# Kernel tuning notes

Hardware: AMD Instinct MI355X
Metric: run time of the kernel (lower is better)

The kernel has to match this reference:

```python
import jax, jax.numpy as jnp
import numpy as np

NEG_SLOPE = 0.2  # PyG GATConv default negative_slope


def _gat_layer(x, src, dst, W, a_src, a_dst, b, num_nodes):
    # x: [N, Fin] -> h: [N, Fout]
    h = x @ W
    # per-node attention logits (heads=1)
    alpha_s = h @ a_src  # [N]
    alpha_d = h @ a_dst  # [N]
    # edge scores e_ij = LeakyReLU(a_src . h_j + a_dst . h_i), j=src, i=dst
    e = alpha_s[src] + alpha_d[dst]
    e = jnp.where(e >= 0, e, NEG_SLOPE * e)
    # segment softmax over edges sharing the same destination node
    e_max = jax.ops.segment_max(e, dst, num_segments=num_nodes)  # [N]
    w = jnp.exp(e - e_max[dst])  # [E]
    denom = jax.ops.segment_sum(w, dst, num_segments=num_nodes)  # [N]
    alpha = w / denom[dst]  # [E]
    # weighted scatter-sum of source messages into destinations
    out = jax.ops.segment_sum(h[src] * alpha[:, None], dst, num_segments=num_nodes)
    return out + b


def _add_self_loops(edge_index, num_nodes):
    loops = jnp.arange(num_nodes, dtype=edge_index.dtype)
    src = jnp.concatenate([edge_index[0], loops])
    dst = jnp.concatenate([edge_index[1], loops])
    return src, dst


def setup_inputs() -> dict:
    key = jax.random.key(0)
    ks = jax.random.split(key, 8)
    N, E, F_in, F_hid, F_out = 50000, 800000, 128, 128, 64
    inp = {
        "node_features": jax.random.normal(ks[0], (N, F_in), dtype=jnp.float32),
        "edge_index": jax.random.randint(ks[1], (2, E), 0, N, dtype=jnp.int32),
        "W1": jax.random.normal(ks[2], (F_in, F_hid), dtype=jnp.float32) / np.sqrt(F_in),
        "a_src1": jax.random.normal(ks[3], (F_hid,), dtype=jnp.float32) / np.sqrt(F_hid),
        "a_dst1": jax.random.normal(ks[4], (F_hid,), dtype=jnp.float32) / np.sqrt(F_hid),
        "b1": jnp.zeros((F_hid,), dtype=jnp.float32),
        "W2": jax.random.normal(ks[5], (F_hid, F_out), dtype=jnp.float32) / np.sqrt(F_hid),
        "a_src2": jax.random.normal(ks[6], (F_out,), dtype=jnp.float32) / np.sqrt(F_out),
        "a_dst2": jax.random.normal(ks[7], (F_out,), dtype=jnp.float32) / np.sqrt(F_out),
        "b2": jnp.zeros((F_out,), dtype=jnp.float32),
    }
    return inp


def reference(node_features, edge_index, W1, a_src1, a_dst1, b1, W2, a_src2, a_dst2, b2):
    num_nodes = node_features.shape[0]
    src, dst = _add_self_loops(edge_index, num_nodes)
    x = _gat_layer(node_features, src, dst, W1, a_src1, a_dst1, b1, num_nodes)
    x = jax.nn.relu(x)
    x = _gat_layer(x, src, dst, W2, a_src2, a_dst2, b2, num_nodes)
    return x
```

## Files before the change

kernel.cpp:

```cpp
#include <hip/hip_runtime.h>
#include <hip/hip_fp16.h>
#include <cstddef>

#define NEG_SLOPE 0.2f
#define TILE 4096
#define CSR_CAP 6144

typedef _Float16 h8 __attribute__((ext_vector_type(8)));
typedef _Float16 h4 __attribute__((ext_vector_type(4)));
typedef float f4 __attribute__((ext_vector_type(4)));

__device__ __forceinline__ float leaky(float x) { return x >= 0.f ? x : NEG_SLOPE * x; }

__device__ __forceinline__ int wave_iscan(int v, int lane) {
#pragma unroll
    for (int off = 1; off < 64; off <<= 1) {
        int t = __shfl_up(v, off);
        if (lane >= off) v += t;
    }
    return v;
}

__global__ __launch_bounds__(256) void prep(
    const float* __restrict__ W1, const float* __restrict__ W2,
    _Float16* __restrict__ W1t, _Float16* __restrict__ W2t,
    int* __restrict__ bfill)
{
    const int b = blockIdx.x;
    const int tid = threadIdx.x;
    if (b == 0) bfill[tid] = 0;
    if (b < 8) {
        for (int i = b * 2048 + tid; i < (b + 1) * 2048; i += 256) {
            int n = i >> 7, k = i & 127;
            W1t[n * 128 + k] = (_Float16)W1[k * 128 + n];
        }
    } else {
        const int bb = b - 8;
        for (int i = bb * 2048 + tid; i < (bb + 1) * 2048; i += 256) {
            int n = i >> 7, k = i & 127;
            W2t[n * 128 + k] = (_Float16)W2[k * 64 + n];
        }
    }
}

__global__ __launch_bounds__(256) void gemm1_scatter(
    const float* __restrict__ x, const _Float16* __restrict__ Wg,
    const float* __restrict__ a_s, const float* __restrict__ a_d,
    _Float16* __restrict__ hh, float* __restrict__ alphaS, float* __restrict__ alphaD,
    int N, int nblk_gemm,
    const int* __restrict__ src, const int* __restrict__ dst,
    int* __restrict__ bfill, unsigned* __restrict__ staging, int cap, int E)
{
    constexpr int K = 128;
    constexpr int LDK = K + 8;
    constexpr int F = 128;
    constexpr int NT = F / 16;

    __shared__ union {
        struct { _Float16 As[64 * LDK]; _Float16 Wt[F * LDK]; } g;
        struct {
            int lcnt[256]; int loff[256]; int gbase[256]; int ws[4];
            unsigned pairs[TILE]; unsigned char bkt[TILE];
        } s;
    } u;

    const int tid = threadIdx.x;

    if (blockIdx.x < (unsigned)nblk_gemm) {
        const int wave = tid >> 6;
        const int lane = tid & 63;
        const int q = lane >> 4;
        const int c = lane & 15;
        const int rowb = blockIdx.x * 64;

        for (int i = tid; i < 64 * (K / 4); i += 256) {
            int r = i >> 5, c4 = i & 31;
            int gr = rowb + r;
            float4 v = (gr < N) ? *(const float4*)(x + (size_t)gr * K + c4 * 4)
                                : make_float4(0.f, 0.f, 0.f, 0.f);
            h4 hv = { (_Float16)v.x, (_Float16)v.y, (_Float16)v.z, (_Float16)v.w };
            *(h4*)(u.g.As + r * LDK + c4 * 4) = hv;
        }
        for (int i = tid; i < F * (K / 8); i += 256) {
            int n = i >> 4, k8 = i & 15;
            *(h8*)(u.g.Wt + n * LDK + k8 * 8) = *(const h8*)(Wg + n * 128 + k8 * 8);
        }
        __syncthreads();

        f4 acc[NT];
#pragma unroll
        for (int nt = 0; nt < NT; nt++) acc[nt] = (f4)0.f;

        const _Float16* aw = u.g.As + (wave * 16 + c) * LDK + q * 8;
#pragma unroll
        for (int kt = 0; kt < 4; kt++) {
            h8 af = *(const h8*)(aw + kt * 32);
#pragma unroll
            for (int nt = 0; nt < NT; nt++) {
                h8 bf = *(const h8*)(u.g.Wt + (nt * 16 + c) * LDK + kt * 32 + q * 8);
                acc[nt] = __builtin_amdgcn_mfma_f32_16x16x32_f16(af, bf, acc[nt], 0, 0, 0);
            }
        }

        float asl[NT], adl[NT];
#pragma unroll
        for (int nt = 0; nt < NT; nt++) {
            asl[nt] = a_s[nt * 16 + c];
            adl[nt] = a_d[nt * 16 + c];
        }
        const int row0 = rowb + wave * 16 + q * 4;
#pragma unroll
        for (int r = 0; r < 4; r++) {
            int row = row0 + r;
            if (row < N) {
                float ps = 0.f, pd = 0.f;
#pragma unroll
                for (int nt = 0; nt < NT; nt++) {
                    float v = acc[nt][r];
                    hh[(size_t)row * F + nt * 16 + c] = (_Float16)v;
                    ps += v * asl[nt];
                    pd += v * adl[nt];
                }
#pragma unroll
                for (int off = 8; off >= 1; off >>= 1) {
                    ps += __shfl_down(ps, off, 16);
                    pd += __shfl_down(pd, off, 16);
                }
                if (c == 0) { alphaS[row] = ps; alphaD[row] = pd; }
            }
        }
    } else {
        const int base = (blockIdx.x - nblk_gemm) * TILE;
        const int vt = min(TILE, E - base);

        u.s.lcnt[tid] = 0;
        __syncthreads();

        int d[TILE / 256], s[TILE / 256], r[TILE / 256];
#pragma unroll
        for (int j = 0; j < TILE / 256; j++) {
            int idx = base + j * 256 + tid;
            if (idx < E) {
                d[j] = dst[idx]; s[j] = src[idx];
                r[j] = atomicAdd(&u.s.lcnt[d[j] >> 8], 1);
            } else d[j] = -1;
        }
        __syncthreads();
        {
            int lane = tid & 63, wid = tid >> 6;
            int v = u.s.lcnt[tid];
            int incl = wave_iscan(v, lane);
            if (lane == 63) u.s.ws[wid] = incl;
            __syncthreads();
            int woff = 0;
            for (int w = 0; w < wid; w++) woff += u.s.ws[w];
            u.s.loff[tid] = woff + incl - v;
        }
        __syncthreads();
        {
            int c = u.s.lcnt[tid];
            if (c > 0) u.s.gbase[tid] = tid * cap + atomicAdd(&bfill[tid], c);
        }
        __syncthreads();
#pragma unroll
        for (int j = 0; j < TILE / 256; j++) {
            if (d[j] >= 0) {
                int b = d[j] >> 8;
                int slot = u.s.loff[b] + r[j];
                u.s.pairs[slot] = ((unsigned)d[j] << 16) | (unsigned)s[j];
                u.s.bkt[slot] = (unsigned char)b;
            }
        }
        __syncthreads();
        for (int slot = tid; slot < vt; slot += 256) {
            int b = u.s.bkt[slot];
            staging[u.s.gbase[b] + (slot - u.s.loff[b])] = u.s.pairs[slot];
        }
    }
}

__global__ __launch_bounds__(1024) void bucket_to_csr(
    const unsigned* __restrict__ staging, const int* __restrict__ bfill,
    int* __restrict__ row_start, int* __restrict__ row_end,
    int* __restrict__ src_sorted, int cap, int N)
{
    __shared__ unsigned lp[CSR_CAP];
    __shared__ int lcnt[256], loff[256], lfill[256];
    __shared__ int ws[4];
    const int tid = threadIdx.x;
    const int b = blockIdx.x;
    const int beg = b * cap;
    const int len = bfill[b];

    if (tid < 256) lcnt[tid] = 0;
    __syncthreads();
    for (int p = tid; p < len; p += 1024) {
        unsigned u = staging[beg + p];
        lp[p] = u;
        atomicAdd(&lcnt[(u >> 16) & 255], 1);
    }
    __syncthreads();
    {
        int lane = tid & 63, wid = tid >> 6;
        int v = 0, incl = 0;
        if (tid < 256) {
            v = lcnt[tid];
            incl = wave_iscan(v, lane);
            if (lane == 63) ws[wid] = incl;
        }
        __syncthreads();
        if (tid < 256) {
            int woff = 0;
            for (int w = 0; w < wid; w++) woff += ws[w];
            int excl = woff + incl - v;
            loff[tid] = excl;
            lfill[tid] = excl;
            int node = (b << 8) + tid;
            if (node < N) { row_start[node] = beg + excl; row_end[node] = beg + excl + v; }
        }
    }
    __syncthreads();
    for (int p = tid; p < len; p += 1024) {
        unsigned u = lp[p];
        int pos = atomicAdd(&lfill[(u >> 16) & 255], 1);
        src_sorted[beg + pos] = (int)(u & 0xFFFFu);
    }
}

__global__ __launch_bounds__(256) void agg1_gemm2(
    const int* __restrict__ row_start, const int* __restrict__ row_end,
    const int* __restrict__ src_sorted, const __half* __restrict__ hh1,
    const float* __restrict__ aS1, const float* __restrict__ aD1,
    const float* __restrict__ b1,
    const _Float16* __restrict__ W2t,
    const float* __restrict__ aS2, const float* __restrict__ aD2,
    _Float16* __restrict__ hh2, float* __restrict__ alphaS2, float* __restrict__ alphaD2,
    int N)
{
    constexpr int K = 128;
    constexpr int LDK = K + 8;
    constexpr int F2 = 64;
    constexpr int NT = F2 / 16;

    __shared__ _Float16 As[64 * LDK];
    __shared__ _Float16 Wt[F2 * LDK];

    const int tid = threadIdx.x;
    const int wave = tid >> 6;
    const int lane = tid & 63;
    const int rowb = blockIdx.x * 64;

    for (int i = tid; i < F2 * (K / 8); i += 256) {
        int n = i >> 4, k8 = i & 15;
        *(h8*)(Wt + n * LDK + k8 * 8) = *(const h8*)(W2t + n * 128 + k8 * 8);
    }

    const int sub = lane >> 4;
    const int l = lane & 15;

    for (int it = 0; it < 16; it++) {
        const int r = wave * 16 + it;
        const int i = rowb + r;
        if (i < N) {
            const float adi = aD1[i];
            const int start = row_start[i];
            const int end = row_end[i];

            float accA[8], accB[8];
#pragma unroll
            for (int q = 0; q < 8; q++) { accA[q] = 0.f; accB[q] = 0.f; }
            float denA = 0.f, denB = 0.f;

            int e = start + sub;
            int s0 = (e + 0 * 4 < end) ? src_sorted[e + 0 * 4] : -1;
            int s1 = (e + 1 * 4 < end) ? src_sorted[e + 1 * 4] : -1;
            int s2 = (e + 2 * 4 < end) ? src_sorted[e + 2 * 4] : -1;
            int s3 = (e + 3 * 4 < end) ? src_sorted[e + 3 * 4] : -1;

            while (s0 >= 0) {
                int eb = e + 16;
                int n0 = (eb + 0 * 4 < end) ? src_sorted[eb + 0 * 4] : -1;
                int n1 = (eb + 1 * 4 < end) ? src_sorted[eb + 1 * 4] : -1;
                int n2 = (eb + 2 * 4 < end) ? src_sorted[eb + 2 * 4] : -1;
                int n3 = (eb + 3 * 4 < end) ? src_sorted[eb + 3 * 4] : -1;

                {
                    float w = __expf(leaky(aS1[s0] + adi));
                    uint4 u = *(const uint4*)(hh1 + (size_t)s0 * 128 + l * 8);
                    const __half2* hp = (const __half2*)&u;
#pragma unroll
                    for (int q = 0; q < 4; q++) {
                        float2 f = __half22float2(hp[q]);
                        accA[q * 2] += w * f.x; accA[q * 2 + 1] += w * f.y;
                    }
                    denA += w;
                }
                if (s1 >= 0) {
                    float w = __expf(leaky(aS1[s1] + adi));
                    uint4 u = *(const uint4*)(hh1 + (size_t)s1 * 128 + l * 8);
                    const __half2* hp = (const __half2*)&u;
#pragma unroll
                    for (int q = 0; q < 4; q++) {
                        float2 f = __half22float2(hp[q]);
                        accB[q * 2] += w * f.x; accB[q * 2 + 1] += w * f.y;
                    }
                    denB += w;
                }
                if (s2 >= 0) {
                    float w = __expf(leaky(aS1[s2] + adi));
                    uint4 u = *(const uint4*)(hh1 + (size_t)s2 * 128 + l * 8);
                    const __half2* hp = (const __half2*)&u;
#pragma unroll
                    for (int q = 0; q < 4; q++) {
                        float2 f = __half22float2(hp[q]);
                        accA[q * 2] += w * f.x; accA[q * 2 + 1] += w * f.y;
                    }
                    denA += w;
                }
                if (s3 >= 0) {
                    float w = __expf(leaky(aS1[s3] + adi));
                    uint4 u = *(const uint4*)(hh1 + (size_t)s3 * 128 + l * 8);
                    const __half2* hp = (const __half2*)&u;
#pragma unroll
                    for (int q = 0; q < 4; q++) {
                        float2 f = __half22float2(hp[q]);
                        accB[q * 2] += w * f.x; accB[q * 2 + 1] += w * f.y;
                    }
                    denB += w;
                }
                e = eb;
                s0 = n0; s1 = n1; s2 = n2; s3 = n3;
            }

            float acc[8];
#pragma unroll
            for (int q = 0; q < 8; q++) acc[q] = accA[q] + accB[q];
            float denom = denA + denB;

#pragma unroll
            for (int off = 32; off >= 16; off >>= 1) {
#pragma unroll
                for (int q = 0; q < 8; q++) acc[q] += __shfl_down(acc[q], off);
                denom += __shfl_down(denom, off);
            }

            if (sub == 0) {
                float wsf = __expf(leaky(aS1[i] + adi));
                uint4 u = *(const uint4*)(hh1 + (size_t)i * 128 + l * 8);
                const __half2* hp = (const __half2*)&u;
                float inv = 1.f / (denom + wsf);
                float4 b0 = *(const float4*)(b1 + l * 8);
                float4 bb1 = *(const float4*)(b1 + l * 8 + 4);
                float o[8];
#pragma unroll
                for (int q = 0; q < 4; q++) {
                    float2 f = __half22float2(hp[q]);
                    o[q * 2]     = (acc[q * 2]     + wsf * f.x) * inv;
                    o[q * 2 + 1] = (acc[q * 2 + 1] + wsf * f.y) * inv;
                }
                o[0] += b0.x; o[1] += b0.y; o[2] += b0.z; o[3] += b0.w;
                o[4] += bb1.x; o[5] += bb1.y; o[6] += bb1.z; o[7] += bb1.w;
                h8 hv;
#pragma unroll
                for (int q = 0; q < 8; q++) hv[q] = (_Float16)fmaxf(o[q], 0.f);
                *(h8*)(As + r * LDK + l * 8) = hv;
            }
        }
    }
    __syncthreads();

    const int q = lane >> 4;
    const int c = lane & 15;

    f4 acc[NT];
#pragma unroll
    for (int nt = 0; nt < NT; nt++) acc[nt] = (f4)0.f;

    const _Float16* aw = As + (wave * 16 + c) * LDK + q * 8;
#pragma unroll
    for (int kt = 0; kt < 4; kt++) {
        h8 af = *(const h8*)(aw + kt * 32);
#pragma unroll
        for (int nt = 0; nt < NT; nt++) {
            h8 bf = *(const h8*)(Wt + (nt * 16 + c) * LDK + kt * 32 + q * 8);
            acc[nt] = __builtin_amdgcn_mfma_f32_16x16x32_f16(af, bf, acc[nt], 0, 0, 0);
        }
    }

    float asl[NT], adl[NT];
#pragma unroll
    for (int nt = 0; nt < NT; nt++) {
        asl[nt] = aS2[nt * 16 + c];
        adl[nt] = aD2[nt * 16 + c];
    }
    const int row0 = rowb + wave * 16 + q * 4;
#pragma unroll
    for (int r = 0; r < 4; r++) {
        int row = row0 + r;
        if (row < N) {
            float ps = 0.f, pd = 0.f;
#pragma unroll
            for (int nt = 0; nt < NT; nt++) {
                float v = acc[nt][r];
                hh2[(size_t)row * F2 + nt * 16 + c] = (_Float16)v;
                ps += v * asl[nt];
                pd += v * adl[nt];
            }
#pragma unroll
            for (int off = 8; off >= 1; off >>= 1) {
                ps += __shfl_down(ps, off, 16);
                pd += __shfl_down(pd, off, 16);
            }
            if (c == 0) { alphaS2[row] = ps; alphaD2[row] = pd; }
        }
    }
}

template <int F, bool RELU, typename OT>
__global__ __launch_bounds__(256) void gat_aggregate(
    const int* __restrict__ row_start, const int* __restrict__ row_end,
    const int* __restrict__ src_sorted, const __half* __restrict__ hh,
    const float* __restrict__ aS, const float* __restrict__ aD,
    const float* __restrict__ bias, OT* __restrict__ out, int N)
{
    constexpr int LPE = F / 8;
    constexpr int EPW = 64 / LPE;

    const int i = blockIdx.x * 4 + (threadIdx.x >> 6);
    if (i >= N) return;
    const int lane = threadIdx.x & 63;
    const int sub = lane / LPE;
    const int l = lane % LPE;

    const float adi = aD[i];
    const int start = row_start[i];
    const int end = row_end[i];

    float accA[8], accB[8];
#pragma unroll
    for (int q = 0; q < 8; q++) { accA[q] = 0.f; accB[q] = 0.f; }
    float denA = 0.f, denB = 0.f;

    int e = start + sub;
    int s0 = (e + 0 * EPW < end) ? src_sorted[e + 0 * EPW] : -1;
    int s1 = (e + 1 * EPW < end) ? src_sorted[e + 1 * EPW] : -1;
    int s2 = (e + 2 * EPW < end) ? src_sorted[e + 2 * EPW] : -1;
    int s3 = (e + 3 * EPW < end) ? src_sorted[e + 3 * EPW] : -1;

    while (s0 >= 0) {
        int eb = e + 4 * EPW;
        int n0 = (eb + 0 * EPW < end) ? src_sorted[eb + 0 * EPW] : -1;
        int n1 = (eb + 1 * EPW < end) ? src_sorted[eb + 1 * EPW] : -1;
        int n2 = (eb + 2 * EPW < end) ? src_sorted[eb + 2 * EPW] : -1;
        int n3 = (eb + 3 * EPW < end) ? src_sorted[eb + 3 * EPW] : -1;

        {
            float w = __expf(leaky(aS[s0] + adi));
            uint4 u = *(const uint4*)(hh + (size_t)s0 * F + l * 8);
            const __half2* hp = (const __half2*)&u;
#pragma unroll
            for (int q = 0; q < 4; q++) {
                float2 f = __half22float2(hp[q]);
                accA[q * 2] += w * f.x; accA[q * 2 + 1] += w * f.y;
            }
            denA += w;
        }
        if (s1 >= 0) {
            float w = __expf(leaky(aS[s1] + adi));
            uint4 u = *(const uint4*)(hh + (size_t)s1 * F + l * 8);
            const __half2* hp = (const __half2*)&u;
#pragma unroll
            for (int q = 0; q < 4; q++) {
                float2 f = __half22float2(hp[q]);
                accB[q * 2] += w * f.x; accB[q * 2 + 1] += w * f.y;
            }
            denB += w;
        }
        if (s2 >= 0) {
            float w = __expf(leaky(aS[s2] + adi));
            uint4 u = *(const uint4*)(hh + (size_t)s2 * F + l * 8);
            const __half2* hp = (const __half2*)&u;
#pragma unroll
            for (int q = 0; q < 4; q++) {
                float2 f = __half22float2(hp[q]);
                accA[q * 2] += w * f.x; accA[q * 2 + 1] += w * f.y;
            }
            denA += w;
        }
        if (s3 >= 0) {
            float w = __expf(leaky(aS[s3] + adi));
            uint4 u = *(const uint4*)(hh + (size_t)s3 * F + l * 8);
            const __half2* hp = (const __half2*)&u;
#pragma unroll
            for (int q = 0; q < 4; q++) {
                float2 f = __half22float2(hp[q]);
                accB[q * 2] += w * f.x; accB[q * 2 + 1] += w * f.y;
            }
            denB += w;
        }
        e = eb;
        s0 = n0; s1 = n1; s2 = n2; s3 = n3;
    }

    float acc[8];
#pragma unroll
    for (int q = 0; q < 8; q++) acc[q] = accA[q] + accB[q];
    float denom = denA + denB;

#pragma unroll
    for (int off = 32; off >= LPE; off >>= 1) {
#pragma unroll
        for (int q = 0; q < 8; q++) acc[q] += __shfl_down(acc[q], off);
        denom += __shfl_down(denom, off);
    }

    if (sub == 0) {
        float wsf = __expf(leaky(aS[i] + adi));
        uint4 u = *(const uint4*)(hh + (size_t)i * F + l * 8);
        const __half2* hp = (const __half2*)&u;
        float inv = 1.f / (denom + wsf);
        float4 b0 = *(const float4*)(bias + l * 8);
        float4 b1 = *(const float4*)(bias + l * 8 + 4);
        float o[8];
#pragma unroll
        for (int q = 0; q < 4; q++) {
            float2 f = __half22float2(hp[q]);
            o[q * 2]     = (acc[q * 2]     + wsf * f.x) * inv;
            o[q * 2 + 1] = (acc[q * 2 + 1] + wsf * f.y) * inv;
        }
        o[0] += b0.x; o[1] += b0.y; o[2] += b0.z; o[3] += b0.w;
        o[4] += b1.x; o[5] += b1.y; o[6] += b1.z; o[7] += b1.w;
        if (RELU) {
#pragma unroll
            for (int q = 0; q < 8; q++) o[q] = fmaxf(o[q], 0.f);
        }
        if constexpr (sizeof(OT) == 2) {
            __half2 qh[4];
            qh[0] = __floats2half2_rn(o[0], o[1]);
            qh[1] = __floats2half2_rn(o[2], o[3]);
            qh[2] = __floats2half2_rn(o[4], o[5]);
            qh[3] = __floats2half2_rn(o[6], o[7]);
            *(uint4*)((__half*)out + (size_t)i * F + l * 8) = *(uint4*)qh;
        } else {
            *(float4*)((float*)out + (size_t)i * F + l * 8)     = make_float4(o[0], o[1], o[2], o[3]);
            *(float4*)((float*)out + (size_t)i * F + l * 8 + 4) = make_float4(o[4], o[5], o[6], o[7]);
        }
    }
}

extern "C" void kernel_launch(void* const* d_in, const int* in_sizes, int n_in,
                              void* d_out, int out_size, void* d_ws, size_t ws_size,
                              hipStream_t stream)
{
    const float* x   = (const float*)d_in[0];
    const int*   ei  = (const int*)d_in[1];
    const float* W1  = (const float*)d_in[2];
    const float* aS1 = (const float*)d_in[3];
    const float* aD1 = (const float*)d_in[4];
    const float* b1  = (const float*)d_in[5];
    const float* W2  = (const float*)d_in[6];
    const float* aS2 = (const float*)d_in[7];
    const float* aD2 = (const float*)d_in[8];
    const float* b2  = (const float*)d_in[9];

    const int K = 128, F1 = 128, F2 = 64;
    const int N = in_sizes[0] / K;
    const int E = in_sizes[1] / 2;
    const int* src = ei;
    const int* dst = ei + E;

    const int Np = (N + 4) & ~3;
    const int NB = (N + 255) >> 8;
    const int nbt = (E + TILE - 1) / TILE;
    const int nblk_gemm = (N + 63) / 64;
    int cap = (((E / NB) * 3) / 2 + 255) & ~255;
    if (cap > CSR_CAP) cap = CSR_CAP;

    char* wsb = (char*)d_ws;
    int* bfill        = (int*)wsb;      wsb += 256 * 4;
    _Float16* W1t     = (_Float16*)wsb; wsb += 128 * 128 * 2;
    _Float16* W2t     = (_Float16*)wsb; wsb += 64 * 128 * 2;
    int* row_start    = (int*)wsb;      wsb += (size_t)Np * 4;
    int* row_end      = (int*)wsb;      wsb += (size_t)Np * 4;
    unsigned* staging = (unsigned*)wsb; wsb += (size_t)NB * CSR_CAP * 4;
    int* src_sorted   = (int*)wsb;      wsb += (size_t)NB * CSR_CAP * 4;
    _Float16* hh1     = (_Float16*)wsb; wsb += (size_t)N * F1 * 2;
    _Float16* hh2     = (_Float16*)wsb; wsb += (size_t)N * F2 * 2;
    float* as_        = (float*)wsb;    wsb += (size_t)Np * 4;
    float* ad_        = (float*)wsb;    wsb += (size_t)Np * 4;
    float* as2_       = (float*)wsb;    wsb += (size_t)Np * 4;
    float* ad2_       = (float*)wsb;    wsb += (size_t)Np * 4;

    dim3 blk(256);

    prep<<<dim3(12), blk, 0, stream>>>(W1, W2, W1t, W2t, bfill);

    gemm1_scatter<<<dim3(nblk_gemm + nbt), blk, 0, stream>>>(
        x, W1t, aS1, aD1, hh1, as_, ad_, N, nblk_gemm,
        src, dst, bfill, staging, cap, E);

    bucket_to_csr<<<dim3(NB), dim3(1024), 0, stream>>>(staging, bfill, row_start, row_end,
                                                       src_sorted, cap, N);

    agg1_gemm2<<<dim3(nblk_gemm), blk, 0, stream>>>(
        row_start, row_end, src_sorted, (const __half*)hh1, as_, ad_, b1,
        W2t, aS2, aD2, hh2, as2_, ad2_, N);

    gat_aggregate<F2, false, float><<<dim3((N + 3) / 4), blk, 0, stream>>>(
        row_start, row_end, src_sorted, (const __half*)hh2, as2_, ad2_, b2,
        (float*)d_out, N);
}
```

Measured before the change: 202.0 us.

## Aggregate one node per wave and replace MFMA tile GEMM with scalar dot

The fused layer-1 aggregation plus layer-2 GEMM kernel now gives each block 4 nodes (one per wave) instead of 64 rows with 16 serial aggregations per wave. This gives far more blocks and better latency hiding for the gathers. The 128x64 projection is now done with FP32 scalar FMAs: each wave takes a 32-wide K slice, reads W2t straight from global memory, and partial sums are reduced through shared memory. The MFMA path is dropped. Separately, the bucket_to_csr block size is cut from 1024 to 512 threads.

```diff
diff --git a/kernel.cpp b/kernel.cpp
--- a/kernel.cpp
+++ b/kernel.cpp
@@ -179,7 +179,7 @@
     }
 }
 
-__global__ __launch_bounds__(1024) void bucket_to_csr(
+__global__ __launch_bounds__(512) void bucket_to_csr(
     const unsigned* __restrict__ staging, const int* __restrict__ bfill,
     int* __restrict__ row_start, int* __restrict__ row_end,
     int* __restrict__ src_sorted, int cap, int N)
@@ -194,7 +194,7 @@
 
     if (tid < 256) lcnt[tid] = 0;
     __syncthreads();
-    for (int p = tid; p < len; p += 1024) {
+    for (int p = tid; p < len; p += 512) {
         unsigned u = staging[beg + p];
         lp[p] = u;
         atomicAdd(&lcnt[(u >> 16) & 255], 1);
@@ -220,14 +220,14 @@
         }
     }
     __syncthreads();
-    for (int p = tid; p < len; p += 1024) {
+    for (int p = tid; p < len; p += 512) {
         unsigned u = lp[p];
         int pos = atomicAdd(&lfill[(u >> 16) & 255], 1);
         src_sorted[beg + pos] = (int)(u & 0xFFFFu);
     }
 }
 
-__global__ __launch_bounds__(256) void agg1_gemm2(
+__global__ __launch_bounds__(256) void agg1_gemm2f(
     const int* __restrict__ row_start, const int* __restrict__ row_end,
     const int* __restrict__ src_sorted, const __half* __restrict__ hh1,
     const float* __restrict__ aS1, const float* __restrict__ aD1,
@@ -237,181 +237,154 @@
     _Float16* __restrict__ hh2, float* __restrict__ alphaS2, float* __restrict__ alphaD2,
     int N)
 {
-    constexpr int K = 128;
-    constexpr int LDK = K + 8;
-    constexpr int F2 = 64;
-    constexpr int NT = F2 / 16;
-
-    __shared__ _Float16 As[64 * LDK];
-    __shared__ _Float16 Wt[F2 * LDK];
-
-    const int tid = threadIdx.x;
-    const int wave = tid >> 6;
-    const int lane = tid & 63;
-    const int rowb = blockIdx.x * 64;
-
-    for (int i = tid; i < F2 * (K / 8); i += 256) {
-        int n = i >> 4, k8 = i & 15;
-        *(h8*)(Wt + n * LDK + k8 * 8) = *(const h8*)(W2t + n * 128 + k8 * 8);
-    }
-
+    __shared__ float x2r[4][128];
+    __shared__ float part[4][4][64];
+
+    const int wave = threadIdx.x >> 6;
+    const int lane = threadIdx.x & 63;
+    const int i = blockIdx.x * 4 + wave;
     const int sub = lane >> 4;
     const int l = lane & 15;
 
-    for (int it = 0; it < 16; it++) {
-        const int r = wave * 16 + it;
-        const int i = rowb + r;
-        if (i < N) {
-            const float adi = aD1[i];
-            const int start = row_start[i];
-            const int end = row_end[i];
-
-            float accA[8], accB[8];
-#pragma unroll
-            for (int q = 0; q < 8; q++) { accA[q] = 0.f; accB[q] = 0.f; }
-            float denA = 0.f, denB = 0.f;
-
-            int e = start + sub;
-            int s0 = (e + 0 * 4 < end) ? src_sorted[e + 0 * 4] : -1;
-            int s1 = (e + 1 * 4 < end) ? src_sorted[e + 1 * 4] : -1;
-            int s2 = (e + 2 * 4 < end) ? src_sorted[e + 2 * 4] : -1;
-            int s3 = (e + 3 * 4 < end) ? src_sorted[e + 3 * 4] : -1;
-
-            while (s0 >= 0) {
-                int eb = e + 16;
-                int n0 = (eb + 0 * 4 < end) ? src_sorted[eb + 0 * 4] : -1;
-                int n1 = (eb + 1 * 4 < end) ? src_sorted[eb + 1 * 4] : -1;
-                int n2 = (eb + 2 * 4 < end) ? src_sorted[eb + 2 * 4] : -1;
-                int n3 = (eb + 3 * 4 < end) ? src_sorted[eb + 3 * 4] : -1;
-
-                {
-                    float w = __expf(leaky(aS1[s0] + adi));
-                    uint4 u = *(const uint4*)(hh1 + (size_t)s0 * 128 + l * 8);
-                    const __half2* hp = (const __half2*)&u;
-#pragma unroll
-                    for (int q = 0; q < 4; q++) {
-                        float2 f = __half22float2(hp[q]);
-                        accA[q * 2] += w * f.x; accA[q * 2 + 1] += w * f.y;
-                    }
-                    denA += w;
-                }
-                if (s1 >= 0) {
-                    float w = __expf(leaky(aS1[s1] + adi));
-                    uint4 u = *(const uint4*)(hh1 + (size_t)s1 * 128 + l * 8);
-                    const __half2* hp = (const __half2*)&u;
-#pragma unroll
-                    for (int q = 0; q < 4; q++) {
-                        float2 f = __half22float2(hp[q]);
-                        accB[q * 2] += w * f.x; accB[q * 2 + 1] += w * f.y;
-                    }
-                    denB += w;
-                }
-                if (s2 >= 0) {
-                    float w = __expf(leaky(aS1[s2] + adi));
-                    uint4 u = *(const uint4*)(hh1 + (size_t)s2 * 128 + l * 8);
-                    const __half2* hp = (const __half2*)&u;
-#pragma unroll
-                    for (int q = 0; q < 4; q++) {
-                        float2 f = __half22float2(hp[q]);
-                        accA[q * 2] += w * f.x; accA[q * 2 + 1] += w * f.y;
-                    }
-                    denA += w;
-                }
-                if (s3 >= 0) {
-                    float w = __expf(leaky(aS1[s3] + adi));
-                    uint4 u = *(const uint4*)(hh1 + (size_t)s3 * 128 + l * 8);
-                    const __half2* hp = (const __half2*)&u;
-#pragma unroll
-                    for (int q = 0; q < 4; q++) {
-                        float2 f = __half22float2(hp[q]);
-                        accB[q * 2] += w * f.x; accB[q * 2 + 1] += w * f.y;
-                    }
-                    denB += w;
-                }
-                e = eb;
-                s0 = n0; s1 = n1; s2 = n2; s3 = n3;
-            }
-
-            float acc[8];
-#pragma unroll
-            for (int q = 0; q < 8; q++) acc[q] = accA[q] + accB[q];
-            float denom = denA + denB;
-
-#pragma unroll
-            for (int off = 32; off >= 16; off >>= 1) {
-#pragma unroll
-                for (int q = 0; q < 8; q++) acc[q] += __shfl_down(acc[q], off);
-                denom += __shfl_down(denom, off);
-            }
-
-            if (sub == 0) {
-                float wsf = __expf(leaky(aS1[i] + adi));
-                uint4 u = *(const uint4*)(hh1 + (size_t)i * 128 + l * 8);
+    if (i < N) {
+        const float adi = aD1[i];
+        const int start = row_start[i];
+        const int end = row_end[i];
+
+        float accA[8], accB[8];
+#pragma unroll
+        for (int q = 0; q < 8; q++) { accA[q] = 0.f; accB[q] = 0.f; }
+        float denA = 0.f, denB = 0.f;
+
+        int e = start + sub;
+        int s0 = (e + 0 * 4 < end) ? src_sorted[e + 0 * 4] : -1;
+        int s1 = (e + 1 * 4 < end) ? src_sorted[e + 1 * 4] : -1;
+        int s2 = (e + 2 * 4 < end) ? src_sorted[e + 2 * 4] : -1;
+        int s3 = (e + 3 * 4 < end) ? src_sorted[e + 3 * 4] : -1;
+
+        while (s0 >= 0) {
+            int eb = e + 16;
+            int n0 = (eb + 0 * 4 < end) ? src_sorted[eb + 0 * 4] : -1;
+            int n1 = (eb + 1 * 4 < end) ? src_sorted[eb + 1 * 4] : -1;
+            int n2 = (eb + 2 * 4 < end) ? src_sorted[eb + 2 * 4] : -1;
+            int n3 = (eb + 3 * 4 < end) ? src_sorted[eb + 3 * 4] : -1;
+
+            {
+                float w = __expf(leaky(aS1[s0] + adi));
+                uint4 u = *(const uint4*)(hh1 + (size_t)s0 * 128 + l * 8);
                 const __half2* hp = (const __half2*)&u;
-                float inv = 1.f / (denom + wsf);
-                float4 b0 = *(const float4*)(b1 + l * 8);
-                float4 bb1 = *(const float4*)(b1 + l * 8 + 4);
-                float o[8];
 #pragma unroll
                 for (int q = 0; q < 4; q++) {
                     float2 f = __half22float2(hp[q]);
-                    o[q * 2]     = (acc[q * 2]     + wsf * f.x) * inv;
-                    o[q * 2 + 1] = (acc[q * 2 + 1] + wsf * f.y) * inv;
+                    accA[q * 2] += w * f.x; accA[q * 2 + 1] += w * f.y;
                 }
-                o[0] += b0.x; o[1] += b0.y; o[2] += b0.z; o[3] += b0.w;
-                o[4] += bb1.x; o[5] += bb1.y; o[6] += bb1.z; o[7] += bb1.w;
-                h8 hv;
-#pragma unroll
-                for (int q = 0; q < 8; q++) hv[q] = (_Float16)fmaxf(o[q], 0.f);
-                *(h8*)(As + r * LDK + l * 8) = hv;
-            }
+                denA += w;
+            }
+            if (s1 >= 0) {
+                float w = __expf(leaky(aS1[s1] + adi));
+                uint4 u = *(const uint4*)(hh1 + (size_t)s1 * 128 + l * 8);
+                const __half2* hp = (const __half2*)&u;
+#pragma unroll
+                for (int q = 0; q < 4; q++) {
+                    float2 f = __half22float2(hp[q]);
+                    accB[q * 2] += w * f.x; accB[q * 2 + 1] += w * f.y;
+                }
+                denB += w;
+            }
+            if (s2 >= 0) {
+                float w = __expf(leaky(aS1[s2] + adi));
+                uint4 u = *(const uint4*)(hh1 + (size_t)s2 * 128 + l * 8);
+                const __half2* hp = (const __half2*)&u;
+#pragma unroll
+                for (int q = 0; q < 4; q++) {
+                    float2 f = __half22float2(hp[q]);
+                    accA[q * 2] += w * f.x; accA[q * 2 + 1] += w * f.y;
+                }
+                denA += w;
+            }
+            if (s3 >= 0) {
+                float w = __expf(leaky(aS1[s3] + adi));
+                uint4 u = *(const uint4*)(hh1 + (size_t)s3 * 128 + l * 8);
+                const __half2* hp = (const __half2*)&u;
+#pragma unroll
+                for (int q = 0; q < 4; q++) {
+                    float2 f = __half22float2(hp[q]);
+                    accB[q * 2] += w * f.x; accB[q * 2 + 1] += w * f.y;
+                }
+                denB += w;
+            }
+            e = eb;
+            s0 = n0; s1 = n1; s2 = n2; s3 = n3;
+        }
+
+        float acc[8];
+#pragma unroll
+        for (int q = 0; q < 8; q++) acc[q] = accA[q] + accB[q];
+        float denom = denA + denB;
+
+#pragma unroll
+        for (int off = 32; off >= 16; off >>= 1) {
+#pragma unroll
+            for (int q = 0; q < 8; q++) acc[q] += __shfl_down(acc[q], off);
+            denom += __shfl_down(denom, off);
+        }
+
+        if (sub == 0) {
+            float wsf = __expf(leaky(aS1[i] + adi));
+            uint4 u = *(const uint4*)(hh1 + (size_t)i * 128 + l * 8);
+            const __half2* hp = (const __half2*)&u;
+            float inv = 1.f / (denom + wsf);
+            float4 b0 = *(const float4*)(b1 + l * 8);
+            float4 bb = *(const float4*)(b1 + l * 8 + 4);
+            float o[8];
+#pragma unroll
+            for (int q = 0; q < 4; q++) {
+                float2 f = __half22float2(hp[q]);
+                o[q * 2]     = (acc[q * 2]     + wsf * f.x) * inv;
+                o[q * 2 + 1] = (acc[q * 2 + 1] + wsf * f.y) * inv;
+            }
+            o[0] += b0.x; o[1] += b0.y; o[2] += b0.z; o[3] += b0.w;
+            o[4] += bb.x; o[5] += bb.y; o[6] += bb.z; o[7] += bb.w;
+#pragma unroll
+            for (int q = 0; q < 8; q++) x2r[wave][l * 8 + q] = fmaxf(o[q], 0.f);
         }
     }
     __syncthreads();
 
-    const int q = lane >> 4;
-    const int c = lane & 15;
-
-    f4 acc[NT];
-#pragma unroll
-    for (int nt = 0; nt < NT; nt++) acc[nt] = (f4)0.f;
-
-    const _Float16* aw = As + (wave * 16 + c) * LDK + q * 8;
-#pragma unroll
-    for (int kt = 0; kt < 4; kt++) {
-        h8 af = *(const h8*)(aw + kt * 32);
-#pragma unroll
-        for (int nt = 0; nt < NT; nt++) {
-            h8 bf = *(const h8*)(Wt + (nt * 16 + c) * LDK + kt * 32 + q * 8);
-            acc[nt] = __builtin_amdgcn_mfma_f32_16x16x32_f16(af, bf, acc[nt], 0, 0, 0);
-        }
-    }
-
-    float asl[NT], adl[NT];
-#pragma unroll
-    for (int nt = 0; nt < NT; nt++) {
-        asl[nt] = aS2[nt * 16 + c];
-        adl[nt] = aD2[nt * 16 + c];
-    }
-    const int row0 = rowb + wave * 16 + q * 4;
-#pragma unroll
-    for (int r = 0; r < 4; r++) {
-        int row = row0 + r;
-        if (row < N) {
-            float ps = 0.f, pd = 0.f;
-#pragma unroll
-            for (int nt = 0; nt < NT; nt++) {
-                float v = acc[nt][r];
-                hh2[(size_t)row * F2 + nt * 16 + c] = (_Float16)v;
-                ps += v * asl[nt];
-                pd += v * adl[nt];
-            }
-#pragma unroll
-            for (int off = 8; off >= 1; off >>= 1) {
-                ps += __shfl_down(ps, off, 16);
-                pd += __shfl_down(pd, off, 16);
-            }
-            if (c == 0) { alphaS2[row] = ps; alphaD2[row] = pd; }
+    float p[4] = {0.f, 0.f, 0.f, 0.f};
+#pragma unroll
+    for (int half = 0; half < 2; half++) {
+        const int k0 = wave * 32 + half * 16;
+        h8 wa = *(const h8*)(W2t + lane * 128 + k0);
+        h8 wb = *(const h8*)(W2t + lane * 128 + k0 + 8);
+#pragma unroll
+        for (int m = 0; m < 4; m++) {
+            float s = 0.f;
+#pragma unroll
+            for (int j = 0; j < 8; j++) s += x2r[m][k0 + j] * (float)wa[j];
+#pragma unroll
+            for (int j = 0; j < 8; j++) s += x2r[m][k0 + 8 + j] * (float)wb[j];
+            p[m] += s;
+        }
+    }
+#pragma unroll
+    for (int m = 0; m < 4; m++) part[wave][m][lane] = p[m];
+    __syncthreads();
+
+    {
+        const int m = wave;
+        const int node = blockIdx.x * 4 + m;
+        if (node < N) {
+            float s = part[0][m][lane] + part[1][m][lane] + part[2][m][lane] + part[3][m][lane];
+            hh2[(size_t)node * 64 + lane] = (_Float16)s;
+            float ps = s * aS2[lane];
+            float pd = s * aD2[lane];
+#pragma unroll
+            for (int off = 32; off >= 1; off >>= 1) {
+                ps += __shfl_down(ps, off);
+                pd += __shfl_down(pd, off);
+            }
+            if (lane == 0) { alphaS2[node] = ps; alphaD2[node] = pd; }
         }
     }
 }
@@ -599,10 +572,10 @@
         x, W1t, aS1, aD1, hh1, as_, ad_, N, nblk_gemm,
         src, dst, bfill, staging, cap, E);
 
-    bucket_to_csr<<<dim3(NB), dim3(1024), 0, stream>>>(staging, bfill, row_start, row_end,
-                                                       src_sorted, cap, N);
-
-    agg1_gemm2<<<dim3(nblk_gemm), blk, 0, stream>>>(
+    bucket_to_csr<<<dim3(NB), dim3(512), 0, stream>>>(staging, bfill, row_start, row_end,
+                                                      src_sorted, cap, N);
+
+    agg1_gemm2f<<<dim3((N + 3) / 4), blk, 0, stream>>>(
         row_start, row_end, src_sorted, (const __half*)hh1, as_, ad_, b1,
         W2t, aS2, aD2, hh2, as2_, ad2_, N);
 
```

Result: no change. 204.8 us (+1.4%).
